# Optimization experiments

Hardware: AMD Instinct MI355X
Metric: run time of the kernel (lower is better)

Reference implementation:

```python
import jax, jax.numpy as jnp
import numpy as np

N_ENT = 200000
N_REL = 500
D_MODEL = 512
BS = 256


def setup_inputs() -> dict:
    key = jax.random.key(0)
    k1, k2, k3, k4, k5, k6 = jax.random.split(key, 6)
    return {
        "s_ent": jax.random.randint(k1, (BS,), 0, N_ENT, dtype=jnp.int32),
        "relation": jax.random.randint(k2, (BS,), 0, N_REL, dtype=jnp.int32),
        "o_ent": jax.random.randint(k3, (BS,), 0, N_ENT, dtype=jnp.int32),
        "time": jax.random.randint(k4, (BS,), 0, 365, dtype=jnp.int32),
        "ent_emb": jax.random.normal(k5, (N_ENT, D_MODEL), dtype=jnp.float32),
        "rel_emb": jax.random.normal(k6, (N_REL, D_MODEL), dtype=jnp.float32),
    }


def reference(s_ent, relation, o_ent, time, ent_emb, rel_emb):
    # test_forward: scores = -||(e_s + r) - E_all||_2 for every entity.
    # Faithful math via the ||a-b||^2 = ||a||^2 - 2 a.b + ||b||^2 GEMM
    # decomposition, avoiding the [bs, n_ent, d] difference tensor.
    cond = ent_emb[s_ent] + rel_emb[relation]          # [bs, d]
    a2 = jnp.sum(cond * cond, axis=-1, keepdims=True)  # [bs, 1]
    b2 = jnp.sum(ent_emb * ent_emb, axis=-1)           # [n_ent]
    ab = jnp.einsum('bd,nd->bn', cond, ent_emb)        # [bs, n_ent]
    d2 = a2 - 2.0 * ab + b2[None, :]
    scores = -jnp.sqrt(jnp.maximum(d2, 1e-12))
    return scores
```

## Files before the change

### kernel.cpp

```cpp
#include <hip/hip_runtime.h>
#include <hip/hip_bf16.h>

typedef __attribute__((ext_vector_type(8))) short short8;
typedef __attribute__((ext_vector_type(4))) float f32x4;

#define D_MODEL 512
#define BN 128
#define NT 16
#define A_TILE 16384
#define B_TILE 16384

__device__ __forceinline__ void gload16(const void* gptr, void* lptr) {
    typedef const __attribute__((address_space(1))) unsigned GT;
    typedef __attribute__((address_space(3))) unsigned LT;
    __builtin_amdgcn_global_load_lds((GT*)gptr, (LT*)lptr, 16, 0, 0);
}

__device__ __forceinline__ short f2bf(float f) {
    unsigned u = __builtin_bit_cast(unsigned, f);
    unsigned r = (u + 0x7fffu + ((u >> 16) & 1u)) >> 16;
    return (short)r;
}

__global__ void prep_kernel(const int* __restrict__ s_ent, const int* __restrict__ rel,
                            const float* __restrict__ ent, const float* __restrict__ relemb,
                            short* __restrict__ condb, float* __restrict__ a2) {
    const int b = blockIdx.x;
    const int t = threadIdx.x;
    const float4 v = *(const float4*)(ent + (size_t)s_ent[b] * D_MODEL + t * 4);
    const float4 w = *(const float4*)(relemb + (size_t)rel[b] * D_MODEL + t * 4);
    float c0 = v.x + w.x, c1 = v.y + w.y, c2 = v.z + w.z, c3 = v.w + w.w;
    float sq = c0 * c0 + c1 * c1 + c2 * c2 + c3 * c3;

    short4 s;
    s.x = f2bf(c0); s.y = f2bf(c1); s.z = f2bf(c2); s.w = f2bf(c3);
    *(short4*)(condb + (size_t)b * D_MODEL + t * 4) = s;

    #pragma unroll
    for (int off = 1; off < 64; off <<= 1) sq += __shfl_xor(sq, off);
    __shared__ float red[2];
    if ((t & 63) == 0) red[t >> 6] = sq;
    __syncthreads();
    if (t == 0) a2[b] = red[0] + red[1];
}

__global__ __launch_bounds__(512, 4)
void score_kernel(const float* __restrict__ ent, const short* __restrict__ condb,
                  const float* __restrict__ a2, float* __restrict__ out, const int n_ent) {
    __shared__ __align__(16) unsigned char lds[2 * A_TILE + 3 * B_TILE];
    unsigned char* Al = lds;
    unsigned char* Bl = lds + 2 * A_TILE;

    const int tid  = threadIdx.x;
    const int lane = tid & 63;
    const int w    = tid >> 6, wm = w >> 1, wn = w & 1;
    const int lrow = lane & 15, g4 = lane >> 4;
    const int nbase = blockIdx.x * BN;

    const int p0 = tid * 16, p1 = p0 + 8192;
    const int ar0 = p0 >> 6, ar1 = p1 >> 6;
    const char* gA0 = (const char*)condb + ar0 * 1024 + ((p0 & 63) ^ ((ar0 & 3) << 4));
    const char* gA1 = (const char*)condb + ar1 * 1024 + ((p1 & 63) ^ ((ar1 & 3) << 4));
    const int br0 = p0 >> 7, br1 = p1 >> 7;
    const long long gr0 = min(nbase + br0, n_ent - 1);
    const long long gr1 = min(nbase + br1, n_ent - 1);
    const char* gB0 = (const char*)ent + gr0 * 2048 + ((p0 & 127) ^ ((br0 & 7) << 4));
    const char* gB1 = (const char*)ent + gr1 * 2048 + ((p1 & 127) ^ ((br1 & 7) << 4));

    int aoff[4], boff0[4], boff1[4];
    #pragma unroll
    for (int f = 0; f < 4; ++f) {
        const int ra = wm * 64 + f * 16 + lrow;
        aoff[f] = ra * 64 + ((g4 * 16) ^ ((ra & 3) << 4));
        const int rb = wn * 64 + f * 16 + lrow;
        const int sw = (rb & 7) << 4;
        boff0[f] = rb * 128 + ((g4 * 32) ^ sw);
        boff1[f] = rb * 128 + ((g4 * 32 + 16) ^ sw);
    }

    f32x4 acc[4][4] = {};
    float sq[4] = {0.f, 0.f, 0.f, 0.f};

    gload16(gA0, Al + p0);
    gload16(gA1, Al + p1);
    gload16(gB0, Bl + p0);
    gload16(gB1, Bl + p1);
    gload16(gB0 + 128, Bl + B_TILE + p0);
    gload16(gB1 + 128, Bl + B_TILE + p1);

    for (int t = 0; t < NT; ++t) {
        if (t == NT - 1) { asm volatile("s_waitcnt vmcnt(0)" ::: "memory"); }
        else             { asm volatile("s_waitcnt vmcnt(2)" ::: "memory"); }
        __builtin_amdgcn_s_barrier();

        if (t + 1 < NT) {
            unsigned char* ad = Al + ((t + 1) & 1) * A_TILE;
            gload16(gA0 + (t + 1) * 64, ad + p0);
            gload16(gA1 + (t + 1) * 64, ad + p1);
        }
        if (t + 2 < NT) {
            unsigned char* bd = Bl + ((t + 2) % 3) * B_TILE;
            gload16(gB0 + (t + 2) * 128, bd + p0);
            gload16(gB1 + (t + 2) * 128, bd + p1);
        }

        const unsigned char* ab = Al + (t & 1) * A_TILE;
        const unsigned char* bb = Bl + (t % 3) * B_TILE;

        short8 af[4];
        #pragma unroll
        for (int fm = 0; fm < 4; ++fm) af[fm] = *(const short8*)(ab + aoff[fm]);

        #pragma unroll
        for (int fn = 0; fn < 4; ++fn) {
            const f32x4 v0 = *(const f32x4*)(bb + boff0[fn]);
            const f32x4 v1 = *(const f32x4*)(bb + boff1[fn]);
            if (wm == 0)
                sq[fn] += v0[0]*v0[0] + v0[1]*v0[1] + v0[2]*v0[2] + v0[3]*v0[3]
                        + v1[0]*v1[0] + v1[1]*v1[1] + v1[2]*v1[2] + v1[3]*v1[3];
            union { __hip_bfloat162 h[4]; short8 s; } cv;
            cv.h[0] = __float22bfloat162_rn(make_float2(v0[0], v0[1]));
            cv.h[1] = __float22bfloat162_rn(make_float2(v0[2], v0[3]));
            cv.h[2] = __float22bfloat162_rn(make_float2(v1[0], v1[1]));
            cv.h[3] = __float22bfloat162_rn(make_float2(v1[2], v1[3]));
            #pragma unroll
            for (int fm = 0; fm < 4; ++fm)
                acc[fm][fn] = __builtin_amdgcn_mfma_f32_16x16x32_bf16(af[fm], cv.s, acc[fm][fn], 0, 0, 0);
        }
    }

    float* b2s = (float*)lds;
    if (wm == 0) {
        #pragma unroll
        for (int fn = 0; fn < 4; ++fn) {
            sq[fn] += __shfl_xor(sq[fn], 16);
            sq[fn] += __shfl_xor(sq[fn], 32);
        }
        if (lane < 16) {
            #pragma unroll
            for (int fn = 0; fn < 4; ++fn) b2s[wn * 64 + fn * 16 + lane] = sq[fn];
        }
    }
    __syncthreads();

    #pragma unroll
    for (int fm = 0; fm < 4; ++fm) {
        const int m0 = wm * 64 + fm * 16 + g4 * 4;
        const f32x4 a2v = *(const f32x4*)(a2 + m0);
        #pragma unroll
        for (int fn = 0; fn < 4; ++fn) {
            const int nl = wn * 64 + fn * 16 + lrow;
            const int ng = nbase + nl;
            if (ng < n_ent) {
                const float b2v = b2s[nl];
                #pragma unroll
                for (int r = 0; r < 4; ++r) {
                    float d2 = a2v[r] - 2.f * acc[fm][fn][r] + b2v;
                    out[(size_t)(m0 + r) * n_ent + ng] = -sqrtf(fmaxf(d2, 1e-12f));
                }
            }
        }
    }
}

extern "C" void kernel_launch(void* const* d_in, const int* in_sizes, int n_in,
                              void* d_out, int out_size, void* d_ws, size_t ws_size,
                              hipStream_t stream) {
    const int*   s_ent  = (const int*)d_in[0];
    const int*   rel    = (const int*)d_in[1];
    const float* ent    = (const float*)d_in[4];
    const float* relemb = (const float*)d_in[5];
    float* out = (float*)d_out;

    const int bs    = in_sizes[0];
    const int n_ent = in_sizes[4] / D_MODEL;

    short* condb = (short*)d_ws;
    float* a2    = (float*)((char*)d_ws + (size_t)bs * D_MODEL * 2);

    prep_kernel<<<bs, 128, 0, stream>>>(s_ent, rel, ent, relemb, condb, a2);

    const int ntiles = (n_ent + BN - 1) / BN;
    score_kernel<<<ntiles, 512, 0, stream>>>(ent, condb, a2, out, n_ent);
}
```

Baseline: 164.6 us.

## Halve entity tile and read query operand directly from global instead of LDS

The entity tile shrinks from 128 to 64 rows and the block drops to 256 threads, with each wave covering 64 query rows. The bf16 query fragments are now loaded straight from global memory each k-step (small, L2-resident) instead of being staged through a double-buffered LDS tile. The main loop is also fully unrolled. This cuts LDS use and barrier-coupled A staging and doubles the block count. In exchange, A reuse across waves now goes through L2, and the hand-written vmcnt waits may interact with the compiler's own waits for the direct A loads.

```diff
diff --git a/kernel.cpp b/kernel.cpp
--- a/kernel.cpp
+++ b/kernel.cpp
@@ -5,21 +5,29 @@
 typedef __attribute__((ext_vector_type(4))) float f32x4;
 
 #define D_MODEL 512
-#define BN 128
+#define BN 64
 #define NT 16
-#define A_TILE 16384
-#define B_TILE 16384
+#define B_TILE 8192
 
-__device__ __forceinline__ void gload16(const void* gptr, void* lptr) {
+__device__ __forceinline__ void gload16(const void* g, void* l) {
     typedef const __attribute__((address_space(1))) unsigned GT;
     typedef __attribute__((address_space(3))) unsigned LT;
-    __builtin_amdgcn_global_load_lds((GT*)gptr, (LT*)lptr, 16, 0, 0);
+    __builtin_amdgcn_global_load_lds((GT*)g, (LT*)l, 16, 0, 0);
 }
 
 __device__ __forceinline__ short f2bf(float f) {
     unsigned u = __builtin_bit_cast(unsigned, f);
     unsigned r = (u + 0x7fffu + ((u >> 16) & 1u)) >> 16;
     return (short)r;
+}
+
+__device__ __forceinline__ short8 cvt8(const f32x4& a, const f32x4& b) {
+    union { __hip_bfloat162 h[4]; short8 s; } u;
+    u.h[0] = __float22bfloat162_rn(make_float2(a[0], a[1]));
+    u.h[1] = __float22bfloat162_rn(make_float2(a[2], a[3]));
+    u.h[2] = __float22bfloat162_rn(make_float2(b[0], b[1]));
+    u.h[3] = __float22bfloat162_rn(make_float2(b[2], b[3]));
+    return u.s;
 }
 
 __global__ void prep_kernel(const int* __restrict__ s_ent, const int* __restrict__ rel,
@@ -44,73 +52,61 @@
     if (t == 0) a2[b] = red[0] + red[1];
 }
 
-__global__ __launch_bounds__(512, 4)
+__global__ __launch_bounds__(256, 4)
 void score_kernel(const float* __restrict__ ent, const short* __restrict__ condb,
                   const float* __restrict__ a2, float* __restrict__ out, const int n_ent) {
-    __shared__ __align__(16) unsigned char lds[2 * A_TILE + 3 * B_TILE];
-    unsigned char* Al = lds;
-    unsigned char* Bl = lds + 2 * A_TILE;
+    __shared__ __align__(16) unsigned char lds[3 * B_TILE];
+    unsigned char* Bl = lds;
 
     const int tid  = threadIdx.x;
     const int lane = tid & 63;
-    const int w    = tid >> 6, wm = w >> 1, wn = w & 1;
+    const int wm   = tid >> 6;
     const int lrow = lane & 15, g4 = lane >> 4;
-    const int nbase = blockIdx.x * BN;
+    const long long nbase = (long long)blockIdx.x * BN;
 
-    const int p0 = tid * 16, p1 = p0 + 8192;
-    const int ar0 = p0 >> 6, ar1 = p1 >> 6;
-    const char* gA0 = (const char*)condb + ar0 * 1024 + ((p0 & 63) ^ ((ar0 & 3) << 4));
-    const char* gA1 = (const char*)condb + ar1 * 1024 + ((p1 & 63) ^ ((ar1 & 3) << 4));
+    const int p0 = tid * 16, p1 = p0 + 4096;
     const int br0 = p0 >> 7, br1 = p1 >> 7;
-    const long long gr0 = min(nbase + br0, n_ent - 1);
-    const long long gr1 = min(nbase + br1, n_ent - 1);
+    const long long gr0 = min(nbase + br0, (long long)(n_ent - 1));
+    const long long gr1 = min(nbase + br1, (long long)(n_ent - 1));
     const char* gB0 = (const char*)ent + gr0 * 2048 + ((p0 & 127) ^ ((br0 & 7) << 4));
     const char* gB1 = (const char*)ent + gr1 * 2048 + ((p1 & 127) ^ ((br1 & 7) << 4));
 
-    int aoff[4], boff0[4], boff1[4];
+    int boff0[4], boff1[4];
     #pragma unroll
     for (int f = 0; f < 4; ++f) {
-        const int ra = wm * 64 + f * 16 + lrow;
-        aoff[f] = ra * 64 + ((g4 * 16) ^ ((ra & 3) << 4));
-        const int rb = wn * 64 + f * 16 + lrow;
+        const int rb = f * 16 + lrow;
         const int sw = (rb & 7) << 4;
         boff0[f] = rb * 128 + ((g4 * 32) ^ sw);
         boff1[f] = rb * 128 + ((g4 * 32 + 16) ^ sw);
     }
 
+    const short* abase = condb + (size_t)(wm * 64 + lrow) * D_MODEL + g4 * 8;
+
     f32x4 acc[4][4] = {};
     float sq[4] = {0.f, 0.f, 0.f, 0.f};
 
-    gload16(gA0, Al + p0);
-    gload16(gA1, Al + p1);
     gload16(gB0, Bl + p0);
     gload16(gB1, Bl + p1);
     gload16(gB0 + 128, Bl + B_TILE + p0);
     gload16(gB1 + 128, Bl + B_TILE + p1);
 
+    #pragma unroll
     for (int t = 0; t < NT; ++t) {
-        if (t == NT - 1) { asm volatile("s_waitcnt vmcnt(0)" ::: "memory"); }
-        else             { asm volatile("s_waitcnt vmcnt(2)" ::: "memory"); }
+        asm volatile("s_waitcnt vmcnt(2)" ::: "memory");
         __builtin_amdgcn_s_barrier();
 
-        if (t + 1 < NT) {
-            unsigned char* ad = Al + ((t + 1) & 1) * A_TILE;
-            gload16(gA0 + (t + 1) * 64, ad + p0);
-            gload16(gA1 + (t + 1) * 64, ad + p1);
-        }
+        const short8 af0 = *(const short8*)(abase + t * 32);
+        const short8 af1 = *(const short8*)(abase + t * 32 + 8192);
+        const short8 af2 = *(const short8*)(abase + t * 32 + 16384);
+        const short8 af3 = *(const short8*)(abase + t * 32 + 24576);
+
         if (t + 2 < NT) {
             unsigned char* bd = Bl + ((t + 2) % 3) * B_TILE;
             gload16(gB0 + (t + 2) * 128, bd + p0);
             gload16(gB1 + (t + 2) * 128, bd + p1);
         }
 
-        const unsigned char* ab = Al + (t & 1) * A_TILE;
         const unsigned char* bb = Bl + (t % 3) * B_TILE;
-
-        short8 af[4];
-        #pragma unroll
-        for (int fm = 0; fm < 4; ++fm) af[fm] = *(const short8*)(ab + aoff[fm]);
-
         #pragma unroll
         for (int fn = 0; fn < 4; ++fn) {
             const f32x4 v0 = *(const f32x4*)(bb + boff0[fn]);
@@ -118,18 +114,15 @@
             if (wm == 0)
                 sq[fn] += v0[0]*v0[0] + v0[1]*v0[1] + v0[2]*v0[2] + v0[3]*v0[3]
                         + v1[0]*v1[0] + v1[1]*v1[1] + v1[2]*v1[2] + v1[3]*v1[3];
-            union { __hip_bfloat162 h[4]; short8 s; } cv;
-            cv.h[0] = __float22bfloat162_rn(make_float2(v0[0], v0[1]));
-            cv.h[1] = __float22bfloat162_rn(make_float2(v0[2], v0[3]));
-            cv.h[2] = __float22bfloat162_rn(make_float2(v1[0], v1[1]));
-            cv.h[3] = __float22bfloat162_rn(make_float2(v1[2], v1[3]));
-            #pragma unroll
-            for (int fm = 0; fm < 4; ++fm)
-                acc[fm][fn] = __builtin_amdgcn_mfma_f32_16x16x32_bf16(af[fm], cv.s, acc[fm][fn], 0, 0, 0);
+            const short8 bf = cvt8(v0, v1);
+            acc[0][fn] = __builtin_amdgcn_mfma_f32_16x16x32_bf16(af0, bf, acc[0][fn], 0, 0, 0);
+            acc[1][fn] = __builtin_amdgcn_mfma_f32_16x16x32_bf16(af1, bf, acc[1][fn], 0, 0, 0);
+            acc[2][fn] = __builtin_amdgcn_mfma_f32_16x16x32_bf16(af2, bf, acc[2][fn], 0, 0, 0);
+            acc[3][fn] = __builtin_amdgcn_mfma_f32_16x16x32_bf16(af3, bf, acc[3][fn], 0, 0, 0);
         }
     }
 
-    float* b2s = (float*)lds;
+    float* b2s = (float*)(lds + B_TILE);
     if (wm == 0) {
         #pragma unroll
         for (int fn = 0; fn < 4; ++fn) {
@@ -138,7 +131,7 @@
         }
         if (lane < 16) {
             #pragma unroll
-            for (int fn = 0; fn < 4; ++fn) b2s[wn * 64 + fn * 16 + lane] = sq[fn];
+            for (int fn = 0; fn < 4; ++fn) b2s[fn * 16 + lane] = sq[fn];
         }
     }
     __syncthreads();
@@ -149,8 +142,8 @@
         const f32x4 a2v = *(const f32x4*)(a2 + m0);
         #pragma unroll
         for (int fn = 0; fn < 4; ++fn) {
-            const int nl = wn * 64 + fn * 16 + lrow;
-            const int ng = nbase + nl;
+            const int nl = fn * 16 + lrow;
+            const long long ng = nbase + nl;
             if (ng < n_ent) {
                 const float b2v = b2s[nl];
                 #pragma unroll
@@ -181,5 +174,5 @@
     prep_kernel<<<bs, 128, 0, stream>>>(s_ent, rel, ent, relemb, condb, a2);
 
     const int ntiles = (n_ent + BN - 1) / BN;
-    score_kernel<<<ntiles, 512, 0, stream>>>(ent, condb, a2, out, n_ent);
+    score_kernel<<<ntiles, 256, 0, stream>>>(ent, condb, a2, out, n_ent);
 }
```

Result: slower. 197.6 us (+20.1%).
